# Kernel optimization log

Measured on AMD Instinct MI355X. Metric: run time of the kernel, lower is better.

The kernel has to match this reference:

```python
import jax, jax.numpy as jnp
import numpy as np

D_MODEL = 1024
STATE_DIM = 256
BATCH = 4
SEQ_LEN = 4096


def setup_inputs() -> dict:
    key = jax.random.key(0)
    k_u, k_B, k_C = jax.random.split(key, 3)
    u = jax.random.normal(k_u, (BATCH, SEQ_LEN, D_MODEL), dtype=jnp.float32)
    # parameters (as in torch init)
    log_lambda = jnp.linspace(2.94, 4.6, STATE_DIM, dtype=jnp.float32)
    # nn.Linear weight shape is [out_features, in_features]
    B_w = jax.random.normal(k_B, (STATE_DIM, D_MODEL), dtype=jnp.float32) / np.sqrt(D_MODEL)
    C_w = jax.random.normal(k_C, (D_MODEL, STATE_DIM), dtype=jnp.float32) / np.sqrt(STATE_DIM)
    D = jnp.ones((D_MODEL,), dtype=jnp.float32)
    return {"u": u, "log_lambda": log_lambda, "B_w": B_w, "C_w": C_w, "D": D}


def reference(u, log_lambda, B_w, C_w, D):
    batch, seq_len, d = u.shape
    # Bu = B(u): [B, L, N]
    Bu = jnp.einsum("bld,nd->bln", u, B_w)
    lam = jax.nn.sigmoid(log_lambda)                     # [N]
    t = jnp.arange(seq_len, dtype=lam.dtype)
    kernel = lam[None, :] ** t[:, None]                  # [L, N]
    # next power of two >= 2*L (static)
    fft_len = 1
    while fft_len < 2 * seq_len:
        fft_len *= 2
    K_hat = jnp.fft.rfft(kernel, n=fft_len, axis=0)      # [F, N]
    Bu_hat = jnp.fft.rfft(Bu, n=fft_len, axis=1)         # [B, F, N]
    h_hat = K_hat[None, :, :] * Bu_hat
    h = jnp.fft.irfft(h_hat, n=fft_len, axis=1)[:, :seq_len, :]  # [B, L, N]
    y = jnp.einsum("bln,dn->bld", h, C_w) + D * u
    return y
```

## Files before the change

kernel.cpp:

```cpp
#include <hip/hip_runtime.h>
#include <hip/hip_bf16.h>

#define D_MODEL 1024
#define STATE_N 256
#define BATCH 4
#define SEQ_LEN 4096
#define M_TOTAL (BATCH * SEQ_LEN)
#define NCHUNK 128
#define CHUNK (SEQ_LEN / NCHUNK)

typedef __attribute__((ext_vector_type(8))) short bf16x8;
typedef __attribute__((ext_vector_type(4))) short s16x4;
typedef __attribute__((ext_vector_type(4))) float f32x4;

static __device__ inline short f2bf(float f) {
    union { float f; unsigned u; } v; v.f = f;
    unsigned r = v.u + 0x7FFFu + ((v.u >> 16) & 1u);
    return (short)(r >> 16);
}
static __device__ inline short f2bf_hw(float f) {
    __hip_bfloat16 h = __float2bfloat16(f);
    return *reinterpret_cast<const short*>(&h);
}
static __device__ inline float bf2f(short s) {
    union { unsigned u; float f; } v;
    v.u = ((unsigned)(unsigned short)s) << 16;
    return v.f;
}
static __device__ inline float sigmoidf(float x) { return 1.0f / (1.0f + expf(-x)); }

#define GLOAD_LDS16(gp, lp)                                                     \
    __builtin_amdgcn_global_load_lds(                                           \
        (const __attribute__((address_space(1))) void*)(gp),                    \
        (__attribute__((address_space(3))) void*)(lp), 16, 0, 0)

#define WAITVM(N) asm volatile("s_waitcnt vmcnt(" #N ")" ::: "memory")
#define BARRIER() do { __builtin_amdgcn_s_barrier(); asm volatile("" ::: "memory"); } while (0)

__global__ void to_bf16_w(const float* __restrict__ Bw, const float* __restrict__ Cw,
                          short* __restrict__ Bwt, short* __restrict__ Cwt) {
    const int g = blockIdx.x * 256 + threadIdx.x;
    const float* s; short* d;
    if (g < 32768) {
        const int col = g & 127, kq = (g >> 7) & 3, kt = (g >> 9) & 31, cb = g >> 14;
        s = Bw + (size_t)(cb * 128 + col) * D_MODEL + kt * 32 + kq * 8;
        d = Bwt + (size_t)g * 8;
    } else {
        const int h = g - 32768;
        const int col = h & 63, ksq = (h >> 6) & 7, t = (h >> 9) & 3, cb = h >> 11;
        s = Cw + (size_t)(cb * 64 + col) * STATE_N + t * 64 + ksq * 8;
        d = Cwt + (size_t)h * 8;
    }
    const f32x4 v0 = *(const f32x4*)s;
    const f32x4 v1 = *(const f32x4*)(s + 4);
    bf16x8 r;
    #pragma unroll
    for (int q = 0; q < 4; ++q) { r[q] = f2bf(v0[q]); r[4 + q] = f2bf(v1[q]); }
    *(bf16x8*)d = r;
}

__global__ __launch_bounds__(256) void gemm1(const float* __restrict__ u,
                                             const short* __restrict__ Bwt,
                                             short* __restrict__ Bu) {
    __shared__ float As[3][64 * 32];
    __shared__ short Bsh[3][4 * 128 * 8];
    const int tid = threadIdx.x;
    const int lane = tid & 63, wave = tid >> 6;
    const int lr = lane & 15, kq = lane >> 4;
    const int wr = wave >> 1, wc = wave & 1;
    const int wg = ((blockIdx.x & 7) << 6) + (blockIdx.x >> 3);
    const int cb = wg & 1, strip = wg >> 1;
    const int m0 = strip * 64, n0 = cb * 128;

    const int aslot0 = wave * 128 + lane, aslot1 = aslot0 + 64;
    const int arow0 = aslot0 >> 3, arow1 = aslot1 >> 3;
    const int ac = lane & 7;
    const float* ag0 = u + (size_t)(m0 + arow0) * D_MODEL + ((ac ^ (arow0 & 7)) << 2);
    const float* ag1 = u + (size_t)(m0 + arow1) * D_MODEL + ((ac ^ (arow1 & 7)) << 2);
    const short* bg = Bwt + ((size_t)cb * 32 * 4 + wave) * 128 * 8;

    f32x4 acc[2][4] = {};

    auto STAGE = [&](int buf, int kt) {
        GLOAD_LDS16(ag0 + kt * 32, (char*)&As[buf][0] + aslot0 * 16);
        GLOAD_LDS16(ag1 + kt * 32, (char*)&As[buf][0] + aslot1 * 16);
        const short* bs = bg + (size_t)kt * 4096;
        GLOAD_LDS16(bs + lane * 8,        (char*)&Bsh[buf][0] + (wave * 128 + lane) * 16);
        GLOAD_LDS16(bs + (64 + lane) * 8, (char*)&Bsh[buf][0] + (wave * 128 + 64 + lane) * 16);
    };
    auto COMPUTE = [&](int buf) {
        bf16x8 af[2];
        #pragma unroll
        for (int i = 0; i < 2; ++i) {
            const int row = wr * 32 + i * 16 + lr;
            const f32x4 a0 = *(const f32x4*)&As[buf][row * 32 + (((kq << 1) ^ (row & 7)) << 2)];
            const f32x4 a1 = *(const f32x4*)&As[buf][row * 32 + ((((kq << 1) | 1) ^ (row & 7)) << 2)];
            #pragma unroll
            for (int e = 0; e < 4; ++e) { af[i][e] = f2bf_hw(a0[e]); af[i][4 + e] = f2bf_hw(a1[e]); }
        }
        bf16x8 bfr[4];
        #pragma unroll
        for (int j = 0; j < 4; ++j)
            bfr[j] = *(const bf16x8*)&Bsh[buf][kq * 1024 + (wc * 64 + j * 16 + lr) * 8];
        #pragma unroll
        for (int i = 0; i < 2; ++i)
            #pragma unroll
            for (int j = 0; j < 4; ++j)
                acc[i][j] = __builtin_amdgcn_mfma_f32_16x16x32_bf16(bfr[j], af[i], acc[i][j], 0, 0, 0);
    };

    STAGE(0, 0);
    STAGE(1, 1);
    #pragma unroll
    for (int t = 0; t < 32; ++t) {
        if (t < 31) { WAITVM(4); } else { WAITVM(0); }
        BARRIER();
        if (t + 2 < 32) STAGE((t + 2) % 3, t + 2);
        COMPUTE(t % 3);
    }

    #pragma unroll
    for (int i = 0; i < 2; ++i) {
        const int m = m0 + wr * 32 + i * 16 + lr;
        #pragma unroll
        for (int j = 0; j < 4; ++j) {
            const int n = n0 + wc * 64 + j * 16 + kq * 4;
            s16x4 st;
            #pragma unroll
            for (int r = 0; r < 4; ++r) st[r] = f2bf(acc[i][j][r]);
            *(s16x4*)(Bu + (size_t)m * STATE_N + n) = st;
        }
    }
}

__global__ __launch_bounds__(256) void gemm2(const short* __restrict__ hbf,
                                             const short* __restrict__ Cwt,
                                             const float* __restrict__ u,
                                             const float* __restrict__ Dv,
                                             float* __restrict__ y) {
    __shared__ short Ash[4][64 * 64];
    __shared__ short Bsh[4][8 * 64 * 8];
    const int tid = threadIdx.x;
    const int lane = tid & 63, wave = tid >> 6;
    const int lr = lane & 15, kq = lane >> 4;
    const int wr = wave >> 1, wc = wave & 1;
    const int wg = ((blockIdx.x & 7) << 9) + (blockIdx.x >> 3);
    const int cb = wg & 15, strip = wg >> 4;
    const int m0 = strip * 64, n0 = cb * 64;

    const int aslot0 = wave * 128 + lane, aslot1 = aslot0 + 64;
    const int arow0 = aslot0 >> 3, arow1 = aslot1 >> 3;
    const int ac = lane & 7;
    const short* ag0 = hbf + (size_t)(m0 + arow0) * STATE_N + ((ac ^ (arow0 & 7)) << 3);
    const short* ag1 = hbf + (size_t)(m0 + arow1) * STATE_N + ((ac ^ (arow1 & 7)) << 3);
    const short* bg = Cwt + (size_t)cb * 4 * 8 * 64 * 8;

    #pragma unroll
    for (int t = 0; t < 4; ++t) {
        GLOAD_LDS16(ag0 + t * 64, (char*)&Ash[t][0] + aslot0 * 16);
        GLOAD_LDS16(ag1 + t * 64, (char*)&Ash[t][0] + aslot1 * 16);
        const short* bs = bg + (size_t)t * 4096;
        GLOAD_LDS16(bs + ((wave * 2 + 0) * 64 + lane) * 8,
                    (char*)&Bsh[t][0] + (wave * 128 + lane) * 16);
        GLOAD_LDS16(bs + ((wave * 2 + 1) * 64 + lane) * 8,
                    (char*)&Bsh[t][0] + (wave * 128 + 64 + lane) * 16);
    }

    f32x4 acc[2][2] = {};
    #pragma unroll
    for (int t = 0; t < 4; ++t) {
        if (t == 0)      { WAITVM(12); }
        else if (t == 1) { WAITVM(8); }
        else if (t == 2) { WAITVM(4); }
        else             { WAITVM(0); }
        BARRIER();
        bf16x8 af[2][2], bfr[2][2];
        #pragma unroll
        for (int ks = 0; ks < 2; ++ks) {
            #pragma unroll
            for (int i = 0; i < 2; ++i) {
                const int row = wr * 32 + i * 16 + lr;
                af[i][ks] = *(const bf16x8*)&Ash[t][row * 64 + ((((ks << 2) | kq) ^ (row & 7)) << 3)];
            }
            #pragma unroll
            for (int j = 0; j < 2; ++j)
                bfr[j][ks] = *(const bf16x8*)&Bsh[t][((ks << 2) | kq) * 512 + (wc * 32 + j * 16 + lr) * 8];
        }
        #pragma unroll
        for (int ks = 0; ks < 2; ++ks)
            #pragma unroll
            for (int i = 0; i < 2; ++i)
                #pragma unroll
                for (int j = 0; j < 2; ++j)
                    acc[i][j] = __builtin_amdgcn_mfma_f32_16x16x32_bf16(bfr[j][ks], af[i][ks], acc[i][j], 0, 0, 0);
    }

    #pragma unroll
    for (int i = 0; i < 2; ++i) {
        const int m = m0 + wr * 32 + i * 16 + lr;
        #pragma unroll
        for (int j = 0; j < 2; ++j) {
            const int n = n0 + wc * 32 + j * 16 + kq * 4;
            const size_t o = (size_t)m * D_MODEL + n;
            const f32x4 uv = *(const f32x4*)(u + o);
            const f32x4 dv = *(const f32x4*)(Dv + n);
            f32x4 rv;
            #pragma unroll
            for (int q = 0; q < 4; ++q) rv[q] = fmaf(dv[q], uv[q], acc[i][j][q]);
            *(f32x4*)(y + o) = rv;
        }
    }
}

__global__ void scan_ends(const short* __restrict__ Bu,
                          const float* __restrict__ log_lambda,
                          float* __restrict__ ends) {
    const int wave = threadIdx.x >> 6, lane = threadIdx.x & 63;
    const int cg = blockIdx.x * 4 + wave;
    const int b = cg >> 7, c = cg & (NCHUNK - 1);
    const int n0 = lane * 4;
    float lam[4], h[4] = {0, 0, 0, 0};
    #pragma unroll
    for (int q = 0; q < 4; ++q) lam[q] = sigmoidf(log_lambda[n0 + q]);
    size_t idx = ((size_t)(b * SEQ_LEN + c * CHUNK)) * STATE_N + n0;
    #pragma unroll
    for (int i = 0; i < CHUNK; ++i) {
        const s16x4 v = *(const s16x4*)(Bu + idx);
        #pragma unroll
        for (int q = 0; q < 4; ++q) h[q] = fmaf(lam[q], h[q], bf2f(v[q]));
        idx += STATE_N;
    }
    f32x4 e;
    #pragma unroll
    for (int q = 0; q < 4; ++q) e[q] = h[q];
    *(f32x4*)(ends + (size_t)cg * STATE_N + n0) = e;
}

__global__ void scan_carry(const float* __restrict__ ends,
                           const float* __restrict__ log_lambda,
                           float* __restrict__ carries) {
    const int n = threadIdx.x;
    const int b = blockIdx.x;
    const float lam = sigmoidf(log_lambda[n]);
    const float lamC = powf(lam, (float)CHUNK);
    float carry = 0.0f;
    #pragma unroll 16
    for (int c = 0; c < NCHUNK; ++c) {
        const size_t o = ((size_t)(b * NCHUNK + c)) * STATE_N + n;
        carries[o] = carry;
        carry = fmaf(lamC, carry, ends[o]);
    }
}

__global__ void scan_fix(const short* __restrict__ Bu,
                         const float* __restrict__ log_lambda,
                         const float* __restrict__ carries,
                         short* __restrict__ hbf) {
    const int wave = threadIdx.x >> 6, lane = threadIdx.x & 63;
    const int cg = blockIdx.x * 4 + wave;
    const int b = cg >> 7, c = cg & (NCHUNK - 1);
    const int n0 = lane * 4;
    float lam[4], h[4];
    #pragma unroll
    for (int q = 0; q < 4; ++q) lam[q] = sigmoidf(log_lambda[n0 + q]);
    const f32x4 cv = *(const f32x4*)(carries + (size_t)cg * STATE_N + n0);
    #pragma unroll
    for (int q = 0; q < 4; ++q) h[q] = cv[q];
    size_t idx = ((size_t)(b * SEQ_LEN + c * CHUNK)) * STATE_N + n0;
    #pragma unroll
    for (int i = 0; i < CHUNK; ++i) {
        const s16x4 v = *(const s16x4*)(Bu + idx);
        s16x4 o;
        #pragma unroll
        for (int q = 0; q < 4; ++q) { h[q] = fmaf(lam[q], h[q], bf2f(v[q])); o[q] = f2bf(h[q]); }
        *(s16x4*)(hbf + idx) = o;
        idx += STATE_N;
    }
}

extern "C" void kernel_launch(void* const* d_in, const int* in_sizes, int n_in,
                              void* d_out, int out_size, void* d_ws, size_t ws_size,
                              hipStream_t stream) {
    const float* u  = (const float*)d_in[0];
    const float* ll = (const float*)d_in[1];
    const float* Bw = (const float*)d_in[2];
    const float* Cw = (const float*)d_in[3];
    const float* Dv = (const float*)d_in[4];
    float* y = (float*)d_out;

    char* ws = (char*)d_ws;
    size_t off = 0;
    short* Bwt = (short*)(ws + off); off += (size_t)STATE_N * D_MODEL * 2;
    short* Cwt = (short*)(ws + off); off += (size_t)D_MODEL * STATE_N * 2;
    short* Bu  = (short*)(ws + off); off += (size_t)M_TOTAL * STATE_N * 2;
    short* hbf = (short*)(ws + off); off += (size_t)M_TOTAL * STATE_N * 2;
    float* ends = (float*)(ws + off); off += (size_t)BATCH * NCHUNK * STATE_N * 4;
    float* carries = (float*)(ws + off);

    to_bf16_w<<<256, 256, 0, stream>>>(Bw, Cw, Bwt, Cwt);
    gemm1<<<512, 256, 0, stream>>>(u, Bwt, Bu);
    scan_ends<<<BATCH * NCHUNK / 4, 256, 0, stream>>>(Bu, ll, ends);
    scan_carry<<<BATCH, STATE_N, 0, stream>>>(ends, ll, carries);
    scan_fix<<<BATCH * NCHUNK / 4, 256, 0, stream>>>(Bu, ll, carries, hbf);
    gemm2<<<4096, 256, 0, stream>>>(hbf, Cwt, u, Dv, y);
}
```

Before: 76.47 us.

## Fuse chunk-end scan into gemm1 epilogue and convert A to bf16 once per tile

Removes the scan_ends kernel. Each gemm1 wave now computes its 32-row chunk's end state as a weighted sum of its accumulators, using a precomputed lambda-power table W, and reduces it with cross-lane shuffles. gemm1 is restructured to load u into registers, convert it to bf16 once, and write it to swizzled LDS, with K-tiles of 64 and double or triple buffering. This avoids the extra pass over Bu and the repeated per-wave fp32-to-bf16 conversion, at the cost of more registers and end states computed from fp32 accumulators rather than rounded bf16 values.

```diff
diff --git a/kernel.cpp b/kernel.cpp
--- a/kernel.cpp
+++ b/kernel.cpp
@@ -18,10 +18,6 @@
     unsigned r = v.u + 0x7FFFu + ((v.u >> 16) & 1u);
     return (short)(r >> 16);
 }
-static __device__ inline short f2bf_hw(float f) {
-    __hip_bfloat16 h = __float2bfloat16(f);
-    return *reinterpret_cast<const short*>(&h);
-}
 static __device__ inline float bf2f(short s) {
     union { unsigned u; float f; } v;
     v.u = ((unsigned)(unsigned short)s) << 16;
@@ -35,20 +31,29 @@
         (__attribute__((address_space(3))) void*)(lp), 16, 0, 0)
 
 #define WAITVM(N) asm volatile("s_waitcnt vmcnt(" #N ")" ::: "memory")
+#define WAITLGKM0 asm volatile("s_waitcnt lgkmcnt(0)" ::: "memory")
 #define BARRIER() do { __builtin_amdgcn_s_barrier(); asm volatile("" ::: "memory"); } while (0)
 
-__global__ void to_bf16_w(const float* __restrict__ Bw, const float* __restrict__ Cw,
-                          short* __restrict__ Bwt, short* __restrict__ Cwt) {
-    const int g = blockIdx.x * 256 + threadIdx.x;
+__global__ void prep(const float* __restrict__ Bw, const float* __restrict__ Cw,
+                     const float* __restrict__ ll,
+                     short* __restrict__ Bwt, short* __restrict__ Cwt,
+                     float* __restrict__ W) {
+    const int bx = blockIdx.x, tid = threadIdx.x;
+    if (bx >= 256) {
+        const int i = bx - 256, n = tid;
+        W[i * 256 + n] = powf(sigmoidf(ll[n]), (float)(31 - i));
+        return;
+    }
+    const int g = bx * 256 + tid;
     const float* s; short* d;
     if (g < 32768) {
-        const int col = g & 127, kq = (g >> 7) & 3, kt = (g >> 9) & 31, cb = g >> 14;
-        s = Bw + (size_t)(cb * 128 + col) * D_MODEL + kt * 32 + kq * 8;
+        const int col = g & 127, kc = (g >> 7) & 7, kt = (g >> 10) & 15, cb = g >> 14;
+        s = Bw + (size_t)(cb * 128 + col) * D_MODEL + kt * 64 + kc * 8;
         d = Bwt + (size_t)g * 8;
     } else {
         const int h = g - 32768;
-        const int col = h & 63, ksq = (h >> 6) & 7, t = (h >> 9) & 3, cb = h >> 11;
-        s = Cw + (size_t)(cb * 64 + col) * STATE_N + t * 64 + ksq * 8;
+        const int col = h & 63, ksq = (h >> 6) & 7, tt = (h >> 9) & 3, cb = h >> 11;
+        s = Cw + (size_t)(cb * 64 + col) * STATE_N + tt * 64 + ksq * 8;
         d = Cwt + (size_t)h * 8;
     }
     const f32x4 v0 = *(const f32x4*)s;
@@ -59,11 +64,13 @@
     *(bf16x8*)d = r;
 }
 
-__global__ __launch_bounds__(256) void gemm1(const float* __restrict__ u,
-                                             const short* __restrict__ Bwt,
-                                             short* __restrict__ Bu) {
-    __shared__ float As[3][64 * 32];
-    __shared__ short Bsh[3][4 * 128 * 8];
+__global__ __launch_bounds__(256, 2) void gemm1(const float* __restrict__ u,
+                                                const short* __restrict__ Bwt,
+                                                const float* __restrict__ W,
+                                                short* __restrict__ Bu,
+                                                float* __restrict__ ends) {
+    __shared__ short Ash[2][64 * 64];
+    __shared__ short Bsh[3][8 * 128 * 8];
     const int tid = threadIdx.x;
     const int lane = tid & 63, wave = tid >> 6;
     const int lr = lane & 15, kq = lane >> 4;
@@ -72,52 +79,83 @@
     const int cb = wg & 1, strip = wg >> 1;
     const int m0 = strip * 64, n0 = cb * 128;
 
-    const int aslot0 = wave * 128 + lane, aslot1 = aslot0 + 64;
-    const int arow0 = aslot0 >> 3, arow1 = aslot1 >> 3;
-    const int ac = lane & 7;
-    const float* ag0 = u + (size_t)(m0 + arow0) * D_MODEL + ((ac ^ (arow0 & 7)) << 2);
-    const float* ag1 = u + (size_t)(m0 + arow1) * D_MODEL + ((ac ^ (arow1 & 7)) << 2);
-    const short* bg = Bwt + ((size_t)cb * 32 * 4 + wave) * 128 * 8;
+    const int a_r = tid >> 4, a_k = (tid & 15) * 4;
+    const float* au = u + (size_t)m0 * D_MODEL + (size_t)a_r * D_MODEL + a_k;
+    const int a_ch = (tid & 15) >> 1, a_half = (tid & 1) * 4;
+    const short* bg = Bwt + (size_t)cb * 16 * 8192;
 
     f32x4 acc[2][4] = {};
-
-    auto STAGE = [&](int buf, int kt) {
-        GLOAD_LDS16(ag0 + kt * 32, (char*)&As[buf][0] + aslot0 * 16);
-        GLOAD_LDS16(ag1 + kt * 32, (char*)&As[buf][0] + aslot1 * 16);
-        const short* bs = bg + (size_t)kt * 4096;
-        GLOAD_LDS16(bs + lane * 8,        (char*)&Bsh[buf][0] + (wave * 128 + lane) * 16);
-        GLOAD_LDS16(bs + (64 + lane) * 8, (char*)&Bsh[buf][0] + (wave * 128 + 64 + lane) * 16);
-    };
-    auto COMPUTE = [&](int buf) {
-        bf16x8 af[2];
-        #pragma unroll
-        for (int i = 0; i < 2; ++i) {
-            const int row = wr * 32 + i * 16 + lr;
-            const f32x4 a0 = *(const f32x4*)&As[buf][row * 32 + (((kq << 1) ^ (row & 7)) << 2)];
-            const f32x4 a1 = *(const f32x4*)&As[buf][row * 32 + ((((kq << 1) | 1) ^ (row & 7)) << 2)];
-            #pragma unroll
-            for (int e = 0; e < 4; ++e) { af[i][e] = f2bf_hw(a0[e]); af[i][4 + e] = f2bf_hw(a1[e]); }
-        }
-        bf16x8 bfr[4];
-        #pragma unroll
-        for (int j = 0; j < 4; ++j)
-            bfr[j] = *(const bf16x8*)&Bsh[buf][kq * 1024 + (wc * 64 + j * 16 + lr) * 8];
-        #pragma unroll
-        for (int i = 0; i < 2; ++i)
+    f32x4 ar0[4], ar1[4], ar2[4];
+
+    #define LOADA(SET, KT)                                                       \
+        do { _Pragma("unroll")                                                   \
+             for (int i = 0; i < 4; ++i)                                         \
+                 SET[i] = *(const f32x4*)(au + (size_t)i * 16 * D_MODEL + (KT) * 64); } while (0)
+    #define WRITEA(BUF, SET)                                                     \
+        do { _Pragma("unroll")                                                   \
+             for (int i = 0; i < 4; ++i) {                                       \
+                 const int row = i * 16 + a_r;                                   \
+                 s16x4 wv;                                                       \
+                 _Pragma("unroll")                                               \
+                 for (int e = 0; e < 4; ++e) wv[e] = f2bf(SET[i][e]);            \
+                 *(s16x4*)&Ash[BUF][(row * 8 + (a_ch ^ (row & 7))) * 8 + a_half] = wv; \
+             } } while (0)
+    #define STAGEB(BUF, KT)                                                      \
+        do { const short* bs = bg + (size_t)(KT) * 8192;                         \
+             _Pragma("unroll")                                                   \
+             for (int q = 0; q < 4; ++q)                                         \
+                 GLOAD_LDS16(bs + (q * 256 + tid) * 8,                           \
+                             (char*)&Bsh[BUF][0] + (q * 256 + wave * 64) * 16); } while (0)
+
+    LOADA(ar0, 0);
+    WAITVM(0);
+    WRITEA(0, ar0);
+    STAGEB(0, 0);
+    LOADA(ar1, 1);
+    STAGEB(1, 1);
+    LOADA(ar2, 2);
+    WAITLGKM0;
+
+    #pragma unroll
+    for (int t = 0; t < 16; ++t) {
+        if (t < 14)      { WAITVM(8); }
+        else if (t == 14){ WAITVM(4); }
+        else             { WAITVM(0); }
+        BARRIER();
+        if (t < 15) {
+            if (((t + 1) % 3) == 0)      WRITEA((t + 1) & 1, ar0);
+            else if (((t + 1) % 3) == 1) WRITEA((t + 1) & 1, ar1);
+            else                         WRITEA((t + 1) & 1, ar2);
+        }
+        bf16x8 af[2][2], bfr[2][4];
+        #pragma unroll
+        for (int ks = 0; ks < 2; ++ks) {
+            #pragma unroll
+            for (int i = 0; i < 2; ++i) {
+                const int row = wr * 32 + i * 16 + lr;
+                af[ks][i] = *(const bf16x8*)&Ash[t & 1][(row * 8 + ((ks * 4 + kq) ^ (row & 7))) * 8];
+            }
             #pragma unroll
             for (int j = 0; j < 4; ++j)
-                acc[i][j] = __builtin_amdgcn_mfma_f32_16x16x32_bf16(bfr[j], af[i], acc[i][j], 0, 0, 0);
-    };
-
-    STAGE(0, 0);
-    STAGE(1, 1);
-    #pragma unroll
-    for (int t = 0; t < 32; ++t) {
-        if (t < 31) { WAITVM(4); } else { WAITVM(0); }
-        BARRIER();
-        if (t + 2 < 32) STAGE((t + 2) % 3, t + 2);
-        COMPUTE(t % 3);
-    }
+                bfr[ks][j] = *(const bf16x8*)&Bsh[t % 3][((ks * 4 + kq) * 128 + wc * 64 + j * 16 + lr) * 8];
+        }
+        if (t + 2 <= 15) STAGEB((t + 2) % 3, t + 2);
+        if (t + 3 <= 15) {
+            if (((t + 3) % 3) == 0)      LOADA(ar0, t + 3);
+            else if (((t + 3) % 3) == 1) LOADA(ar1, t + 3);
+            else                         LOADA(ar2, t + 3);
+        }
+        #pragma unroll
+        for (int ks = 0; ks < 2; ++ks)
+            #pragma unroll
+            for (int i = 0; i < 2; ++i)
+                #pragma unroll
+                for (int j = 0; j < 4; ++j)
+                    acc[i][j] = __builtin_amdgcn_mfma_f32_16x16x32_bf16(bfr[ks][j], af[ks][i], acc[i][j], 0, 0, 0);
+    }
+    #undef LOADA
+    #undef WRITEA
+    #undef STAGEB
 
     #pragma unroll
     for (int i = 0; i < 2; ++i) {
@@ -129,6 +167,34 @@
             #pragma unroll
             for (int r = 0; r < 4; ++r) st[r] = f2bf(acc[i][j][r]);
             *(s16x4*)(Bu + (size_t)m * STATE_N + n) = st;
+        }
+    }
+
+    float part[4][4];
+    #pragma unroll
+    for (int j = 0; j < 4; ++j) {
+        const int nb = n0 + wc * 64 + j * 16 + kq * 4;
+        const f32x4 w0 = *(const f32x4*)(W + (size_t)lr * 256 + nb);
+        const f32x4 w1 = *(const f32x4*)(W + (size_t)(16 + lr) * 256 + nb);
+        #pragma unroll
+        for (int r = 0; r < 4; ++r)
+            part[j][r] = w0[r] * acc[0][j][r] + w1[r] * acc[1][j][r];
+    }
+    #pragma unroll
+    for (int m = 1; m <= 8; m <<= 1)
+        #pragma unroll
+        for (int j = 0; j < 4; ++j)
+            #pragma unroll
+            for (int r = 0; r < 4; ++r)
+                part[j][r] += __shfl_xor(part[j][r], m, 64);
+    if (lr == 0) {
+        const int cg = strip * 2 + wr;
+        #pragma unroll
+        for (int j = 0; j < 4; ++j) {
+            f32x4 e;
+            #pragma unroll
+            for (int r = 0; r < 4; ++r) e[r] = part[j][r];
+            *(f32x4*)(ends + (size_t)cg * STATE_N + n0 + wc * 64 + j * 16 + kq * 4) = e;
         }
     }
 }
@@ -212,30 +278,6 @@
     }
 }
 
-__global__ void scan_ends(const short* __restrict__ Bu,
-                          const float* __restrict__ log_lambda,
-                          float* __restrict__ ends) {
-    const int wave = threadIdx.x >> 6, lane = threadIdx.x & 63;
-    const int cg = blockIdx.x * 4 + wave;
-    const int b = cg >> 7, c = cg & (NCHUNK - 1);
-    const int n0 = lane * 4;
-    float lam[4], h[4] = {0, 0, 0, 0};
-    #pragma unroll
-    for (int q = 0; q < 4; ++q) lam[q] = sigmoidf(log_lambda[n0 + q]);
-    size_t idx = ((size_t)(b * SEQ_LEN + c * CHUNK)) * STATE_N + n0;
-    #pragma unroll
-    for (int i = 0; i < CHUNK; ++i) {
-        const s16x4 v = *(const s16x4*)(Bu + idx);
-        #pragma unroll
-        for (int q = 0; q < 4; ++q) h[q] = fmaf(lam[q], h[q], bf2f(v[q]));
-        idx += STATE_N;
-    }
-    f32x4 e;
-    #pragma unroll
-    for (int q = 0; q < 4; ++q) e[q] = h[q];
-    *(f32x4*)(ends + (size_t)cg * STATE_N + n0) = e;
-}
-
 __global__ void scan_carry(const float* __restrict__ ends,
                            const float* __restrict__ log_lambda,
                            float* __restrict__ carries) {
@@ -292,14 +334,14 @@
     size_t off = 0;
     short* Bwt = (short*)(ws + off); off += (size_t)STATE_N * D_MODEL * 2;
     short* Cwt = (short*)(ws + off); off += (size_t)D_MODEL * STATE_N * 2;
+    float* W   = (float*)(ws + off); off += (size_t)32 * STATE_N * 4;
     short* Bu  = (short*)(ws + off); off += (size_t)M_TOTAL * STATE_N * 2;
     short* hbf = (short*)(ws + off); off += (size_t)M_TOTAL * STATE_N * 2;
     float* ends = (float*)(ws + off); off += (size_t)BATCH * NCHUNK * STATE_N * 4;
     float* carries = (float*)(ws + off);
 
-    to_bf16_w<<<256, 256, 0, stream>>>(Bw, Cw, Bwt, Cwt);
-    gemm1<<<512, 256, 0, stream>>>(u, Bwt, Bu);
-    scan_ends<<<BATCH * NCHUNK / 4, 256, 0, stream>>>(Bu, ll, ends);
+    prep<<<288, 256, 0, stream>>>(Bw, Cw, ll, Bwt, Cwt, W);
+    gemm1<<<512, 256, 0, stream>>>(u, Bwt, W, Bu, ends);
     scan_carry<<<BATCH, STATE_N, 0, stream>>>(ends, ll, carries);
     scan_fix<<<BATCH * NCHUNK / 4, 256, 0, stream>>>(Bu, ll, carries, hbf);
     gemm2<<<4096, 256, 0, stream>>>(hbf, Cwt, u, Dv, y);
```

New measurement: 70.77 us. 1.08x faster.
